# Kernel optimization log

Hardware: AMD Instinct MI355X
Metric: run time of the kernel (lower is better)

## Reference

```python
import jax, jax.numpy as jnp
import numpy as np

SEQ, WORD, EMBED, NHEAD = 2048, 1024, 128, 16


def setup_inputs() -> dict:
    key = jax.random.key(0)
    ks = jax.random.split(key, 6)
    sw = 1.0 / np.sqrt(WORD)  # xavier-ish scale for linear weights
    sp = 1.0 / np.sqrt(EMBED * NHEAD)
    return {
        "x": jax.random.normal(ks[0], (SEQ, WORD), jnp.float32),
        "Wq": jax.random.normal(ks[1], (NHEAD, WORD, EMBED), jnp.float32) * sw,
        "bq": jnp.zeros((NHEAD, EMBED), jnp.float32),
        "Wk": jax.random.normal(ks[2], (NHEAD, WORD, EMBED), jnp.float32) * sw,
        "bk": jnp.zeros((NHEAD, EMBED), jnp.float32),
        "Wv": jax.random.normal(ks[3], (NHEAD, WORD, EMBED), jnp.float32) * sw,
        "bv": jnp.zeros((NHEAD, EMBED), jnp.float32),
        "proj": jax.random.normal(ks[4], (NHEAD * EMBED, EMBED), jnp.float32) * sp,
    }


def reference(x, Wq, bq, Wk, bk, Wv, bv, proj):
    # Batched-head equivalent of the per-head Attention ModuleList loop.
    # x: [S, W]; Wq/Wk/Wv: [H, W, E]; b*: [H, E]; proj: [H*E, E]
    Q = jnp.einsum("sw,hwe->hse", x, Wq) + bq[:, None, :]
    K = jnp.einsum("sw,hwe->hse", x, Wk) + bk[:, None, :]
    V = jnp.einsum("sw,hwe->hse", x, Wv) + bv[:, None, :]
    scale = 1.0 / jnp.sqrt(jnp.asarray(EMBED, x.dtype))
    scores = jnp.einsum("hqe,hke->hqk", Q, K) * scale  # [H, S, S]
    attn = jax.nn.softmax(scores, axis=-1)
    Z = jnp.einsum("hqk,hke->hqe", attn, V)  # [H, S, E]
    # torch.cat([...], dim=1): per-head outputs side-by-side -> [S, H*E]
    Z_s = jnp.transpose(Z, (1, 0, 2)).reshape(x.shape[0], -1)
    return Z_s @ proj  # [S, E]
```

## Files before the change

kernel.cpp:

```cpp
#include <hip/hip_runtime.h>
#include <stdint.h>

#define GAS __attribute__((address_space(1)))
#define LAS __attribute__((address_space(3)))

typedef unsigned short u16;
typedef __attribute__((ext_vector_type(8))) __bf16 bf16x8;
typedef __attribute__((ext_vector_type(4))) float f32x4;

#define SEQ 2048
#define WORD 1024
#define EMBED 128
#define NHEAD 16

__device__ __forceinline__ u16 f2b(float f) {
  return __builtin_bit_cast(u16, (__bf16)f);
}

__global__ __launch_bounds__(256) void cast_x_kernel(const float* __restrict__ x,
                                                     u16* __restrict__ xb) {
  int i = (blockIdx.x * 256 + threadIdx.x) * 4;
  float4 v = *(const float4*)(x + i);
  ushort4 o;
  o.x = f2b(v.x); o.y = f2b(v.y); o.z = f2b(v.z); o.w = f2b(v.w);
  *(ushort4*)(xb + i) = o;
}

__global__ __launch_bounds__(256) void transpose_cast_kernel(
    const float* __restrict__ s0, const float* __restrict__ s1,
    const float* __restrict__ s2, u16* __restrict__ d0, u16* __restrict__ d1,
    u16* __restrict__ d2, int R, int C, long stride, int zsel) {
  __shared__ float tile[32][33];
  const float* s;
  u16* d;
  if (zsel) {
    int z = blockIdx.z;
    int wsel = z >> 4, hh = z & 15;
    s = (wsel == 0 ? s0 : wsel == 1 ? s1 : s2) + (long)hh * stride;
    d = (wsel == 0 ? d0 : wsel == 1 ? d1 : d2) + (long)hh * stride;
  } else {
    s = s0; d = d0;
  }
  int r0 = blockIdx.x * 32, c0 = blockIdx.y * 32;
  int tx = threadIdx.x & 31, ty = threadIdx.x >> 5;
#pragma unroll
  for (int i = 0; i < 4; ++i)
    tile[ty + i * 8][tx] = s[(long)(r0 + ty + i * 8) * C + c0 + tx];
  __syncthreads();
#pragma unroll
  for (int i = 0; i < 4; ++i)
    d[(long)(c0 + ty + i * 8) * R + r0 + tx] = f2b(tile[tx][ty + i * 8]);
}

template <typename OUT>
__device__ __forceinline__ void gemm128(const u16* __restrict__ A, const u16* __restrict__ B,
                                        OUT* __restrict__ C, int lda, int ldb, int ldc,
                                        int ksteps, const float* biasN, const float* biasM,
                                        float scale) {
  __shared__ u16 lA[128 * 64];
  __shared__ u16 lB[128 * 64];
  const int tid = threadIdx.x;
  const int l = tid & 63, w = tid >> 6;
  const int quad = l >> 4, ln = l & 15;
  const int wm = w >> 1, wn = w & 1;
  f32x4 acc[4][4] = {};
  for (int ks = 0; ks < ksteps; ++ks) {
    const u16* Ak = A + ks * 64;
    const u16* Bk = B + ks * 64;
    __syncthreads();
#pragma unroll
    for (int i = 0; i < 4; ++i) {
      int idx = w * 256 + i * 64 + l;
      int r = idx >> 3, cp = idx & 7;
      int cg = cp ^ (r & 7);
      __builtin_amdgcn_global_load_lds((const GAS void*)(Ak + (long)r * lda + cg * 8),
                                       (LAS void*)(lA + (w * 256 + i * 64) * 8), 16, 0, 0);
      __builtin_amdgcn_global_load_lds((const GAS void*)(Bk + (long)r * ldb + cg * 8),
                                       (LAS void*)(lB + (w * 256 + i * 64) * 8), 16, 0, 0);
    }
    __syncthreads();
    bf16x8 af[2][4], bfv[2][4];
#pragma unroll
    for (int kc = 0; kc < 2; ++kc) {
#pragma unroll
      for (int i = 0; i < 4; ++i) {
        int c = kc * 4 + quad;
        int rm = wm * 64 + i * 16 + ln;
        af[kc][i] = *(const bf16x8*)(lA + rm * 64 + ((c ^ (rm & 7)) * 8));
        int rn = wn * 64 + i * 16 + ln;
        bfv[kc][i] = *(const bf16x8*)(lB + rn * 64 + ((c ^ (rn & 7)) * 8));
      }
    }
#pragma unroll
    for (int kc = 0; kc < 2; ++kc)
#pragma unroll
      for (int i = 0; i < 4; ++i)
#pragma unroll
        for (int j = 0; j < 4; ++j)
          acc[i][j] = __builtin_amdgcn_mfma_f32_16x16x32_bf16(af[kc][i], bfv[kc][j],
                                                              acc[i][j], 0, 0, 0);
  }
#pragma unroll
  for (int i = 0; i < 4; ++i) {
#pragma unroll
    for (int j = 0; j < 4; ++j) {
      int row0 = wm * 64 + i * 16 + quad * 4;
      int col = wn * 64 + j * 16 + ln;
      float bn = biasN ? biasN[col] : 0.f;
#pragma unroll
      for (int reg = 0; reg < 4; ++reg) {
        int row = row0 + reg;
        float bm = biasM ? biasM[row] : 0.f;
        float v = (acc[i][j][reg] + bn + bm) * scale;
        if constexpr (sizeof(OUT) == 2)
          C[(long)row * ldc + col] = (OUT)f2b(v);
        else
          C[(long)row * ldc + col] = v;
      }
    }
  }
}

__global__ __launch_bounds__(256, 3) void qkv_gemm_kernel(
    const u16* __restrict__ xb, const u16* __restrict__ Wqt, const u16* __restrict__ Wkt,
    const u16* __restrict__ Wvt, const float* __restrict__ bq, const float* __restrict__ bk,
    const float* __restrict__ bv, u16* __restrict__ Q, u16* __restrict__ Kb,
    u16* __restrict__ Vt) {
  const int t = blockIdx.x;
  const int h = blockIdx.y;
  const int which = blockIdx.z;
  const float qscale = 0.12753042123789493f;
  if (which == 0) {
    gemm128<u16>(xb + t * 128 * WORD, Wqt + h * EMBED * WORD,
                 Q + h * SEQ * EMBED + t * 128 * EMBED, WORD, WORD, EMBED,
                 WORD / 64, bq + h * EMBED, nullptr, qscale);
  } else if (which == 1) {
    gemm128<u16>(xb + t * 128 * WORD, Wkt + h * EMBED * WORD,
                 Kb + h * SEQ * EMBED + t * 128 * EMBED, WORD, WORD, EMBED,
                 WORD / 64, bk + h * EMBED, nullptr, 1.f);
  } else {
    gemm128<u16>(Wvt + h * EMBED * WORD, xb + t * 128 * WORD,
                 Vt + h * EMBED * SEQ + t * 128, WORD, WORD, SEQ,
                 WORD / 64, nullptr, bv + h * EMBED, 1.f);
  }
}

__global__ __launch_bounds__(512, 2) void attn_kernel(const u16* __restrict__ Q,
                                                      const u16* __restrict__ K,
                                                      const u16* __restrict__ V,
                                                      u16* __restrict__ Zs) {
  __shared__ u16 lKV[2][4 * 8192];
  __shared__ u16 lP[8 * 16 * 72];
  const int bid = blockIdx.x;
  const int swz = (bid & 7) * 32 + (bid >> 3);
  const int h = swz >> 4, qb = swz & 15;
  const int tid = threadIdx.x;
  const int l = tid & 63, w = tid >> 6, quad = l >> 4, ln = l & 15;
  const int wr = w >> 1, wk = w & 1;
  const u16* Qh = Q + h * SEQ * EMBED;
  const u16* Kh = K + h * SEQ * EMBED;
  const u16* Vh = V + h * EMBED * SEQ;
  u16* Pw = lP + w * (16 * 72);
  const int q0 = qb * 128 + wr * 32;

  auto stage = [&](int buf, int sup) {
#pragma unroll
    for (int j = 0; j < 4; ++j) {
      int kb = j >> 1;
      int cb = (j & 1) * 512 + w * 64;
      int c = cb + l;
      int rk = c >> 4, cgk = (c & 15) ^ (rk & 15);
      __builtin_amdgcn_global_load_lds(
          (const GAS void*)(Kh + (sup * 128 + kb * 64 + rk) * EMBED + cgk * 8),
          (LAS void*)(&lKV[buf][kb * 8192 + cb * 8]), 16, 0, 0);
      int rv = c >> 3, cgv = (c & 7) ^ (rv & 7);
      __builtin_amdgcn_global_load_lds(
          (const GAS void*)(Vh + rv * SEQ + sup * 128 + kb * 64 + cgv * 8),
          (LAS void*)(&lKV[buf][16384 + kb * 8192 + cb * 8]), 16, 0, 0);
    }
  };

  bf16x8 qf[2][4];
#pragma unroll
  for (int rs = 0; rs < 2; ++rs)
#pragma unroll
    for (int kc = 0; kc < 4; ++kc)
      qf[rs][kc] = *(const bf16x8*)(Qh + (q0 + rs * 16 + ln) * EMBED + kc * 32 + quad * 8);

  const __bf16 ov = (ln == 0) ? (__bf16)1.0f : (__bf16)0.0f;
  const bf16x8 onesf = {ov, ov, ov, ov, ov, ov, ov, ov};

  f32x4 oacc[2][8] = {};
  f32x4 lacc[2] = {};

  stage(0, 0);
  asm volatile("s_waitcnt vmcnt(0)" ::: "memory");
  __builtin_amdgcn_s_barrier();
  __builtin_amdgcn_sched_barrier(0);

  int cur = 0;
#pragma unroll 1
  for (int sup = 0; sup < SEQ / 128; ++sup) {
    if (sup + 1 < SEQ / 128) {
      stage(cur ^ 1, sup + 1);
      asm volatile("s_waitcnt vmcnt(8)" ::: "memory");
    } else {
      asm volatile("s_waitcnt vmcnt(0)" ::: "memory");
    }
    __builtin_amdgcn_s_barrier();
    __builtin_amdgcn_sched_barrier(0);

    const u16* myK = &lKV[cur][wk * 8192];
    const u16* myV = &lKV[cur][16384 + wk * 8192];

    f32x4 sacc[2][4] = {};
#pragma unroll
    for (int kc = 0; kc < 4; ++kc) {
      bf16x8 kf[4];
#pragma unroll
      for (int ns = 0; ns < 4; ++ns) {
        int kr = ns * 16 + ln;
        kf[ns] = *(const bf16x8*)(myK + kr * 128 + (((kc * 4 + quad) ^ (kr & 15)) * 8));
      }
      __builtin_amdgcn_s_setprio(1);
#pragma unroll
      for (int ns = 0; ns < 4; ++ns)
#pragma unroll
        for (int rs = 0; rs < 2; ++rs)
          sacc[rs][ns] = __builtin_amdgcn_mfma_f32_16x16x32_bf16(qf[rs][kc], kf[ns],
                                                                 sacc[rs][ns], 0, 0, 0);
      __builtin_amdgcn_s_setprio(0);
    }
    bf16x8 vf[2][8];
#pragma unroll
    for (int kc = 0; kc < 2; ++kc)
#pragma unroll
      for (int es = 0; es < 8; ++es) {
        int er = es * 16 + ln;
        vf[kc][es] = *(const bf16x8*)(myV + er * 64 + (((kc * 4 + quad) ^ (er & 7)) * 8));
      }
#pragma unroll
    for (int rs = 0; rs < 2; ++rs) {
#pragma unroll
      for (int ns = 0; ns < 4; ++ns)
#pragma unroll
        for (int r = 0; r < 4; ++r)
          Pw[(quad * 4 + r) * 72 + ns * 16 + ln] = f2b(exp2f(sacc[rs][ns][r]));
#pragma unroll
      for (int kc = 0; kc < 2; ++kc) {
        bf16x8 pa = *(const bf16x8*)(Pw + ln * 72 + kc * 32 + quad * 8);
        __builtin_amdgcn_s_setprio(1);
#pragma unroll
        for (int es = 0; es < 8; ++es)
          oacc[rs][es] = __builtin_amdgcn_mfma_f32_16x16x32_bf16(pa, vf[kc][es],
                                                                 oacc[rs][es], 0, 0, 0);
        lacc[rs] = __builtin_amdgcn_mfma_f32_16x16x32_bf16(pa, onesf, lacc[rs], 0, 0, 0);
        __builtin_amdgcn_s_setprio(0);
      }
    }
    __builtin_amdgcn_sched_barrier(0);
    __builtin_amdgcn_s_barrier();
    cur ^= 1;
  }
  __syncthreads();
  float* lO = (float*)lKV;
  if (wk == 1) {
#pragma unroll
    for (int rs = 0; rs < 2; ++rs) {
#pragma unroll
      for (int es = 0; es < 8; ++es)
#pragma unroll
        for (int r = 0; r < 4; ++r)
          lO[wr * 4224 + (rs * 16 + quad * 4 + r) * 132 + es * 16 + ln] = oacc[rs][es][r];
      if (ln == 0)
#pragma unroll
        for (int r = 0; r < 4; ++r)
          lO[wr * 4224 + (rs * 16 + quad * 4 + r) * 132 + 128] = lacc[rs][r];
    }
  }
  __syncthreads();
  if (wk == 0) {
#pragma unroll
    for (int rs = 0; rs < 2; ++rs)
#pragma unroll
      for (int r = 0; r < 4; ++r) {
        int lrow = rs * 16 + quad * 4 + r;
        float lsum = __shfl(lacc[rs][r], l & 48) + lO[wr * 4224 + lrow * 132 + 128];
        float rl = 1.f / lsum;
        int srow = q0 + lrow;
#pragma unroll
        for (int es = 0; es < 8; ++es) {
          float o = oacc[rs][es][r] + lO[wr * 4224 + lrow * 132 + es * 16 + ln];
          Zs[(long)srow * (NHEAD * EMBED) + h * EMBED + es * 16 + ln] = f2b(o * rl);
        }
      }
  }
}

__global__ __launch_bounds__(256, 2) void final_gemm_kernel(const u16* __restrict__ Zs,
                                                            const u16* __restrict__ projT,
                                                            float* __restrict__ pbuf) {
  const int t = blockIdx.x;
  const int kc = blockIdx.y;
  gemm128<float>(Zs + (long)t * 128 * (NHEAD * EMBED) + kc * 256, projT + kc * 256,
                 pbuf + (long)kc * SEQ * EMBED + t * 128 * EMBED,
                 NHEAD * EMBED, NHEAD * EMBED, EMBED, 4, nullptr, nullptr, 1.f);
}

__global__ __launch_bounds__(256) void reduce_kernel(const float* __restrict__ pbuf,
                                                     float* __restrict__ out) {
  int i = (blockIdx.x * 256 + threadIdx.x) * 4;
  float4 s = {0.f, 0.f, 0.f, 0.f};
#pragma unroll
  for (int kc = 0; kc < 8; ++kc) {
    float4 v = *(const float4*)(pbuf + (long)kc * SEQ * EMBED + i);
    s.x += v.x; s.y += v.y; s.z += v.z; s.w += v.w;
  }
  *(float4*)(out + i) = s;
}

extern "C" void kernel_launch(void* const* d_in, const int* in_sizes, int n_in,
                              void* d_out, int out_size, void* d_ws, size_t ws_size,
                              hipStream_t stream) {
  const float* x    = (const float*)d_in[0];
  const float* Wq   = (const float*)d_in[1];
  const float* bq   = (const float*)d_in[2];
  const float* Wk   = (const float*)d_in[3];
  const float* bk   = (const float*)d_in[4];
  const float* Wv   = (const float*)d_in[5];
  const float* bv   = (const float*)d_in[6];
  const float* proj = (const float*)d_in[7];
  float* out = (float*)d_out;

  char* ws = (char*)d_ws;
  u16* xb    = (u16*)(ws);
  u16* Wqt   = (u16*)(ws + (4L << 20));
  u16* Wkt   = (u16*)(ws + (8L << 20));
  u16* Wvt   = (u16*)(ws + (12L << 20));
  u16* projT = (u16*)(ws + (16L << 20));
  u16* Qm    = (u16*)(ws + (17L << 20));
  u16* Km    = (u16*)(ws + (26L << 20));
  u16* Vt    = (u16*)(ws + (35L << 20));
  u16* Zs    = (u16*)(ws + (44L << 20));
  float* pbuf = (float*)(ws);

  cast_x_kernel<<<dim3(SEQ * WORD / 1024), dim3(256), 0, stream>>>(x, xb);
  transpose_cast_kernel<<<dim3(WORD / 32, EMBED / 32, 48), dim3(256), 0, stream>>>(
      Wq, Wk, Wv, Wqt, Wkt, Wvt, WORD, EMBED, (long)WORD * EMBED, 1);
  transpose_cast_kernel<<<dim3(SEQ / 32, EMBED / 32, 1), dim3(256), 0, stream>>>(
      proj, nullptr, nullptr, projT, nullptr, nullptr, SEQ, EMBED, 0, 0);

  qkv_gemm_kernel<<<dim3(16, NHEAD, 3), dim3(256), 0, stream>>>(
      xb, Wqt, Wkt, Wvt, bq, bk, bv, Qm, Km, Vt);

  attn_kernel<<<dim3(256), dim3(512), 0, stream>>>(Qm, Km, Vt, Zs);

  final_gemm_kernel<<<dim3(16, 8), dim3(256), 0, stream>>>(Zs, projT, pbuf);
  reduce_kernel<<<dim3(SEQ * EMBED / 1024), dim3(256), 0, stream>>>(pbuf, out);
}
```

Baseline: 194.9 us.

## Keep P in registers via permlane swaps and load V directly from global

The attention kernel computes S transposed (K as the A operand), so exp'd probabilities can be packed to bf16 and rearranged with permlane32/16 swaps into the MFMA A-operand layout, removing the LDS round-trip for P. Row sums are accumulated in registers and reduced with shuffles instead of an extra ones-MFMA. V fragments are now loaded straight from global memory into registers rather than staged through LDS, halving the LDS staging traffic and changing the waitcnt pipeline. This trades LDS traffic and MFMA work for more in-flight global loads and register pressure.

```diff
diff --git a/kernel.cpp b/kernel.cpp
--- a/kernel.cpp
+++ b/kernel.cpp
@@ -7,6 +7,8 @@
 typedef unsigned short u16;
 typedef __attribute__((ext_vector_type(8))) __bf16 bf16x8;
 typedef __attribute__((ext_vector_type(4))) float f32x4;
+typedef __attribute__((ext_vector_type(2))) unsigned int u32x2;
+typedef __attribute__((ext_vector_type(4))) unsigned int u32x4;
 
 #define SEQ 2048
 #define WORD 1024
@@ -15,6 +17,12 @@
 
 __device__ __forceinline__ u16 f2b(float f) {
   return __builtin_bit_cast(u16, (__bf16)f);
+}
+
+__device__ __forceinline__ unsigned cvt_pk_bf16(float lo, float hi) {
+  unsigned r;
+  asm("v_cvt_pk_bf16_f32 %0, %1, %2" : "=v"(r) : "v"(lo), "v"(hi));
+  return r;
 }
 
 __global__ __launch_bounds__(256) void cast_x_kernel(const float* __restrict__ x,
@@ -149,8 +157,8 @@
                                                       const u16* __restrict__ K,
                                                       const u16* __restrict__ V,
                                                       u16* __restrict__ Zs) {
-  __shared__ u16 lKV[2][4 * 8192];
-  __shared__ u16 lP[8 * 16 * 72];
+  __shared__ __align__(16) char smem[67584];
+  u16* lK = (u16*)smem;
   const int bid = blockIdx.x;
   const int swz = (bid & 7) * 32 + (bid >> 3);
   const int h = swz >> 4, qb = swz & 15;
@@ -160,7 +168,6 @@
   const u16* Qh = Q + h * SEQ * EMBED;
   const u16* Kh = K + h * SEQ * EMBED;
   const u16* Vh = V + h * EMBED * SEQ;
-  u16* Pw = lP + w * (16 * 72);
   const int q0 = qb * 128 + wr * 32;
 
   auto stage = [&](int buf, int sup) {
@@ -172,11 +179,7 @@
       int rk = c >> 4, cgk = (c & 15) ^ (rk & 15);
       __builtin_amdgcn_global_load_lds(
           (const GAS void*)(Kh + (sup * 128 + kb * 64 + rk) * EMBED + cgk * 8),
-          (LAS void*)(&lKV[buf][kb * 8192 + cb * 8]), 16, 0, 0);
-      int rv = c >> 3, cgv = (c & 7) ^ (rv & 7);
-      __builtin_amdgcn_global_load_lds(
-          (const GAS void*)(Vh + rv * SEQ + sup * 128 + kb * 64 + cgv * 8),
-          (LAS void*)(&lKV[buf][16384 + kb * 8192 + cb * 8]), 16, 0, 0);
+          (LAS void*)(lK + buf * 16384 + kb * 8192 + cb * 8), 16, 0, 0);
     }
   };
 
@@ -187,31 +190,32 @@
     for (int kc = 0; kc < 4; ++kc)
       qf[rs][kc] = *(const bf16x8*)(Qh + (q0 + rs * 16 + ln) * EMBED + kc * 32 + quad * 8);
 
-  const __bf16 ov = (ln == 0) ? (__bf16)1.0f : (__bf16)0.0f;
-  const bf16x8 onesf = {ov, ov, ov, ov, ov, ov, ov, ov};
-
   f32x4 oacc[2][8] = {};
-  f32x4 lacc[2] = {};
+  float rsum[2] = {0.f, 0.f};
 
   stage(0, 0);
-  asm volatile("s_waitcnt vmcnt(0)" ::: "memory");
-  __builtin_amdgcn_s_barrier();
-  __builtin_amdgcn_sched_barrier(0);
 
   int cur = 0;
 #pragma unroll 1
   for (int sup = 0; sup < SEQ / 128; ++sup) {
+    bf16x8 vf[2][8];
+#pragma unroll
+    for (int kc = 0; kc < 2; ++kc)
+#pragma unroll
+      for (int es = 0; es < 8; ++es)
+        vf[kc][es] = *(const bf16x8*)(Vh + (long)(es * 16 + ln) * SEQ + sup * 128 +
+                                      wk * 64 + kc * 32 + quad * 8);
+    __builtin_amdgcn_sched_barrier(0);
     if (sup + 1 < SEQ / 128) {
       stage(cur ^ 1, sup + 1);
-      asm volatile("s_waitcnt vmcnt(8)" ::: "memory");
+      asm volatile("s_waitcnt vmcnt(20)" ::: "memory");
     } else {
-      asm volatile("s_waitcnt vmcnt(0)" ::: "memory");
+      asm volatile("s_waitcnt vmcnt(16)" ::: "memory");
     }
     __builtin_amdgcn_s_barrier();
     __builtin_amdgcn_sched_barrier(0);
 
-    const u16* myK = &lKV[cur][wk * 8192];
-    const u16* myV = &lKV[cur][16384 + wk * 8192];
+    const u16* myK = lK + cur * 16384 + wk * 8192;
 
     f32x4 sacc[2][4] = {};
 #pragma unroll
@@ -227,43 +231,61 @@
       for (int ns = 0; ns < 4; ++ns)
 #pragma unroll
         for (int rs = 0; rs < 2; ++rs)
-          sacc[rs][ns] = __builtin_amdgcn_mfma_f32_16x16x32_bf16(qf[rs][kc], kf[ns],
+          sacc[rs][ns] = __builtin_amdgcn_mfma_f32_16x16x32_bf16(kf[ns], qf[rs][kc],
                                                                  sacc[rs][ns], 0, 0, 0);
       __builtin_amdgcn_s_setprio(0);
     }
-    bf16x8 vf[2][8];
-#pragma unroll
-    for (int kc = 0; kc < 2; ++kc)
-#pragma unroll
-      for (int es = 0; es < 8; ++es) {
-        int er = es * 16 + ln;
-        vf[kc][es] = *(const bf16x8*)(myV + er * 64 + (((kc * 4 + quad) ^ (er & 7)) * 8));
-      }
+    asm volatile("s_waitcnt lgkmcnt(0)" ::: "memory");
+    __builtin_amdgcn_sched_barrier(0);
+    __builtin_amdgcn_s_barrier();
+
 #pragma unroll
     for (int rs = 0; rs < 2; ++rs) {
+      float p[4][4];
 #pragma unroll
       for (int ns = 0; ns < 4; ++ns)
 #pragma unroll
-        for (int r = 0; r < 4; ++r)
-          Pw[(quad * 4 + r) * 72 + ns * 16 + ln] = f2b(exp2f(sacc[rs][ns][r]));
+        for (int r = 0; r < 4; ++r) p[ns][r] = exp2f(sacc[rs][ns][r]);
+      float s0 = (p[0][0] + p[0][1]) + (p[0][2] + p[0][3]);
+      float s1 = (p[1][0] + p[1][1]) + (p[1][2] + p[1][3]);
+      float s2 = (p[2][0] + p[2][1]) + (p[2][2] + p[2][3]);
+      float s3 = (p[3][0] + p[3][1]) + (p[3][2] + p[3][3]);
+      rsum[rs] += (s0 + s1) + (s2 + s3);
 #pragma unroll
       for (int kc = 0; kc < 2; ++kc) {
-        bf16x8 pa = *(const bf16x8*)(Pw + ln * 72 + kc * 32 + quad * 8);
+        int n0 = kc * 2, n1 = kc * 2 + 1;
+        unsigned a0 = cvt_pk_bf16(p[n0][0], p[n0][1]);
+        unsigned a1 = cvt_pk_bf16(p[n0][2], p[n0][3]);
+        unsigned b0 = cvt_pk_bf16(p[n1][0], p[n1][1]);
+        unsigned b1 = cvt_pk_bf16(p[n1][2], p[n1][3]);
+        u32x2 t0 = __builtin_amdgcn_permlane32_swap(a0, b0, false, false);
+        u32x2 u0 = __builtin_amdgcn_permlane16_swap(t0.x, t0.y, false, false);
+        u32x2 t1 = __builtin_amdgcn_permlane32_swap(a1, b1, false, false);
+        u32x2 u1 = __builtin_amdgcn_permlane16_swap(t1.x, t1.y, false, false);
+        u32x4 paw = {u0.x, u1.x, u0.y, u1.y};
+        bf16x8 pa = __builtin_bit_cast(bf16x8, paw);
         __builtin_amdgcn_s_setprio(1);
 #pragma unroll
         for (int es = 0; es < 8; ++es)
           oacc[rs][es] = __builtin_amdgcn_mfma_f32_16x16x32_bf16(pa, vf[kc][es],
                                                                  oacc[rs][es], 0, 0, 0);
-        lacc[rs] = __builtin_amdgcn_mfma_f32_16x16x32_bf16(pa, onesf, lacc[rs], 0, 0, 0);
         __builtin_amdgcn_s_setprio(0);
       }
     }
-    __builtin_amdgcn_sched_barrier(0);
-    __builtin_amdgcn_s_barrier();
     cur ^= 1;
   }
+
+  float srl[2][4];
+#pragma unroll
+  for (int rs = 0; rs < 2; ++rs) {
+    float t = rsum[rs] + __shfl(rsum[rs], l ^ 16);
+    t = t + __shfl(t, l ^ 32);
+#pragma unroll
+    for (int r = 0; r < 4; ++r) srl[rs][r] = __shfl(t, quad * 4 + r);
+  }
+
   __syncthreads();
-  float* lO = (float*)lKV;
+  float* lO = (float*)smem;
   if (wk == 1) {
 #pragma unroll
     for (int rs = 0; rs < 2; ++rs) {
@@ -275,7 +297,7 @@
       if (ln == 0)
 #pragma unroll
         for (int r = 0; r < 4; ++r)
-          lO[wr * 4224 + (rs * 16 + quad * 4 + r) * 132 + 128] = lacc[rs][r];
+          lO[wr * 4224 + (rs * 16 + quad * 4 + r) * 132 + 128] = srl[rs][r];
     }
   }
   __syncthreads();
@@ -285,7 +307,7 @@
 #pragma unroll
       for (int r = 0; r < 4; ++r) {
         int lrow = rs * 16 + quad * 4 + r;
-        float lsum = __shfl(lacc[rs][r], l & 48) + lO[wr * 4224 + lrow * 132 + 128];
+        float lsum = srl[rs][r] + lO[wr * 4224 + lrow * 132 + 128];
         float rl = 1.f / lsum;
         int srow = q0 + lrow;
 #pragma unroll
```

Result: slower. 228.8 us (+17.4%).
